# Performance work log

Measured on AMD Instinct MI355X. Metric: run time of the kernel, lower is better.

## Reference

```python
import jax, jax.numpy as jnp
import numpy as np

B = 32            # batch size
N = 100           # n_nodes (== MAX_N_NODES here)
MAXN = 100        # MAX_N_NODES
H = 256           # HIDDEN_DIM_FEATURES_EXTRACTOR
HA = 1024         # HIDDEN_DIM_ACTOR
HC = 512          # HIDDEN_DIM_CRITIC
K_ACTIVE = 5000   # exact number of active mask entries per batch element


def setup_inputs() -> dict:
    key = jax.random.key(0)
    ks = jax.random.split(key, 16)
    feat = jax.random.normal(ks[0], (B, N + 1, H), jnp.float32)
    # mask: exactly K_ACTIVE ones among N*N per batch row (dim == K for all rows)
    rng = np.random.default_rng(0)
    mask = np.zeros((B, N * N), np.float32)
    for i in range(B):
        mask[i, rng.choice(N * N, size=K_ACTIVE, replace=False)] = 1.0
    mask = jnp.asarray(mask).reshape(B, N, N)
    ext_mask = jnp.concatenate([jnp.zeros((B, 1, N), jnp.float32), mask], axis=1)  # [B, N+1, N]
    embedded_features = jnp.concatenate([feat, ext_mask], axis=2)  # [B, N+1, H+N]

    def lin(k, fi, fo):
        s = 1.0 / np.sqrt(fi)
        return (jax.random.uniform(k, (fi, fo), jnp.float32, -s, s),
                jax.random.uniform(jax.random.fold_in(k, 1), (fo,), jnp.float32, -s, s))

    aW1, ab1 = lin(ks[1], 3 * H, HA)
    aW2, ab2 = lin(ks[2], HA, HA)
    aW3, ab3 = lin(ks[3], HA, 1)
    cW1, cb1 = lin(ks[4], H, HC)
    cW2, cb2 = lin(ks[5], HC, HC)
    cW3, cb3 = lin(ks[6], HC, 1)
    return dict(embedded_features=embedded_features,
                aW1=aW1, ab1=ab1, aW2=aW2, ab2=ab2, aW3=aW3, ab3=ab3,
                cW1=cW1, cb1=cb1, cW2=cW2, cb2=cb2, cW3=cW3, cb3=cb3,
                K=K_ACTIVE)


def reference(embedded_features, aW1, ab1, aW2, ab2, aW3, ab3,
              cW1, cb1, cW2, cb2, cW3, cb3, K):
    # decompose features
    gn = embedded_features[:, :, :H]
    ext_mask = embedded_features[:, :, H:]
    g = gn[:, :1, :]                      # [B,1,H] graph embedding
    nodes = gn[:, 1:, :]                  # [B,N,H] node embeddings
    mask = ext_mask[:, 1:, :].reshape(B, -1)  # [B, N*N]

    # indexes of active pairs (stable top_k -> ascending indices among ones, like nonzero)
    _, idx = jax.lax.top_k(mask, K)       # [B,K] int32
    idx1 = idx // N
    idx2 = idx % N
    n1 = jnp.take_along_axis(nodes, idx1[:, :, None], axis=1)  # [B,K,H]
    n2 = jnp.take_along_axis(nodes, idx2[:, :, None], axis=1)  # [B,K,H]
    pairs = jnp.concatenate([jnp.broadcast_to(g, (B, K, H)), n1, n2], axis=-1)  # [B,K,3H]

    # actor MLP (tanh hidden activations)
    h = jnp.tanh(pairs @ aW1 + ab1)
    h = jnp.tanh(h @ aW2 + ab2)
    logits = h @ aW3 + ab3                # [B,K,1]
    pi = jax.nn.softmax(logits, axis=1)   # softmax over the K gathered pairs

    # scatter back into padded grid
    shaped = jnp.zeros((B, N * N), pi.dtype).at[jnp.arange(B)[:, None], idx].set(pi[..., 0])
    filled = jnp.zeros((B, MAXN, MAXN), pi.dtype).at[:, :N, :N].set(shaped.reshape(B, N, N))
    filled = filled.reshape(B, MAXN * MAXN)

    # critic MLP on graph embedding
    hv = jnp.tanh(g @ cW1 + cb1)
    hv = jnp.tanh(hv @ cW2 + cb2)
    value = hv @ cW3 + cb3                # [B,1,1]
    return filled, value
```

## Files before the change

kernel.cpp:

```cpp
#include <hip/hip_runtime.h>
#include <stdint.h>

#define AS1 __attribute__((address_space(1)))
#define AS3 __attribute__((address_space(3)))

typedef __bf16 bf16x8 __attribute__((ext_vector_type(8)));
typedef float  f32x4  __attribute__((ext_vector_type(4)));
typedef int    i32x4  __attribute__((ext_vector_type(4)));
typedef int    i32x8  __attribute__((ext_vector_type(8)));
typedef float  f32x16 __attribute__((ext_vector_type(16)));

__device__ __forceinline__ float tanh_fast(float x){
    float e = __expf(2.0f * x);
    return 1.0f - 2.0f * __builtin_amdgcn_rcpf(e + 1.0f);
}

__device__ __forceinline__ unsigned int cvt_pk_bf16(float lo, float hi){
    unsigned int r;
    asm("v_cvt_pk_bf16_f32 %0, %1, %2" : "=v"(r) : "v"(lo), "v"(hi));
    return r;
}
__device__ __forceinline__ unsigned short f2bf1(float f){
    return (unsigned short)(cvt_pk_bf16(f, f) & 0xffffu);
}

__device__ __forceinline__ float exp2_fast(float x){
#if defined(__has_builtin) && __has_builtin(__builtin_amdgcn_exp2f)
    return __builtin_amdgcn_exp2f(x);
#else
    float r; asm("v_exp_f32 %0, %1" : "=v"(r) : "v"(x)); return r;
#endif
}

__device__ __forceinline__ float q4s(float s){
    float a  = fabsf(s);
    float m1 = fmaf(a, 3.931945f, 0.0039260f);
    float m2 = fmaf(a, 3.428853f, 0.1414056f);
    float m3 = fmaf(a, 1.610679f, 1.3191011f);
    float g  = fminf(fminf(m1, m2), fminf(m3, 4.0f));
    return __builtin_copysignf(g, s);
}

template<int SEL>
__device__ __forceinline__ unsigned int pk4(unsigned int old, float a, float b){
#if defined(__has_builtin) && __has_builtin(__builtin_amdgcn_cvt_scalef32_pk_fp4_f32)
    return __builtin_amdgcn_cvt_scalef32_pk_fp4_f32(old, a, b, 1.0f, SEL);
#else
    float fa = fabsf(a), fb = fabsf(b);
    unsigned int ma = fa < 0.25f ? 0u : fa < 0.75f ? 1u : fa < 1.25f ? 2u :
                      fa < 1.75f ? 3u : fa < 2.5f  ? 4u : fa < 3.5f  ? 5u :
                      fa < 5.0f  ? 6u : 7u;
    unsigned int mb = fb < 0.25f ? 0u : fb < 0.75f ? 1u : fb < 1.25f ? 2u :
                      fb < 1.75f ? 3u : fb < 2.5f  ? 4u : fb < 3.5f  ? 5u :
                      fb < 5.0f  ? 6u : 7u;
    ma |= (a < 0.0f ? 8u : 0u); mb |= (b < 0.0f ? 8u : 0u);
    return old | ((ma | (mb << 4)) << (8 * SEL));
#endif
}

__device__ __forceinline__ i32x8 lo4(i32x4 a){
    return __builtin_shufflevector(a, a, 0, 1, 2, 3, -1, -1, -1, -1);
}

#define B2F(u, lo, hi) { lo = __uint_as_float((u) << 16); hi = __uint_as_float((u) & 0xffff0000u); }

__device__ __forceinline__ unsigned int mk4(uint4 qa, uint4 qb){
    float a0, a1, b0, b1; unsigned int dd = 0;
    B2F(qa.x, a0, a1); B2F(qb.x, b0, b1); dd = pk4<0>(dd, q4s(a0 + b0), q4s(a1 + b1));
    B2F(qa.y, a0, a1); B2F(qb.y, b0, b1); dd = pk4<1>(dd, q4s(a0 + b0), q4s(a1 + b1));
    B2F(qa.z, a0, a1); B2F(qb.z, b0, b1); dd = pk4<2>(dd, q4s(a0 + b0), q4s(a1 + b1));
    B2F(qa.w, a0, a1); B2F(qb.w, b0, b1); dd = pk4<3>(dd, q4s(a0 + b0), q4s(a1 + b1));
    return dd;
}
__device__ __forceinline__ i32x4 mkaf(uint4 a0, uint4 a1, uint4 a2, uint4 a3,
                                      uint4 b0, uint4 b1, uint4 b2, uint4 b3){
    i32x4 f = {(int)mk4(a0, b0), (int)mk4(a1, b1), (int)mk4(a2, b2), (int)mk4(a3, b3)};
    return f;
}

__global__ __launch_bounds__(256) void k_prep(
    const float* __restrict__ ef, const float* __restrict__ aW1, const float* __restrict__ ab1,
    const float* __restrict__ aW2,
    const float* __restrict__ cW1, const float* __restrict__ cb1,
    const float* __restrict__ cW2, const float* __restrict__ cb2,
    const float* __restrict__ cW3, const float* __restrict__ cb3,
    unsigned short* __restrict__ w1b, float* __restrict__ g1,
    int* __restrict__ pairs, unsigned char* __restrict__ w2b,
    float* __restrict__ out)
{
    __shared__ float gsl[256], h1[512], h2[512], wred[4];
    __shared__ int lcnt;
    int blk = blockIdx.x, t = threadIdx.x;

    if (blk < 256){
        int s = blk >> 7, cb = (blk >> 3) & 15, kt = blk & 7;
        int w = t >> 6, lane = t & 63, quad = lane >> 4, n = lane & 15;
        int c = cb * 64 + w * 16 + n;
        const float* src = aW1 + (size_t)(256 + s * 256 + kt * 32 + quad * 8) * 1024 + c;
        unsigned int d[4];
#pragma unroll
        for (int j = 0; j < 4; ++j)
            d[j] = cvt_pk_bf16(src[(size_t)(2*j) * 1024], src[(size_t)(2*j+1) * 1024]);
        *(uint4*)(w1b + (size_t)blk * 2048 + t * 8) = make_uint4(d[0], d[1], d[2], d[3]);
    } else if (blk < 384){
        int bi = blk - 256, b = bi >> 2, q = bi & 3;
        gsl[t] = ef[(size_t)b * 35956 + t];
        __syncthreads();
        int o = q * 256 + t;
        float s = ab1[o];
#pragma unroll 8
        for (int i = 0; i < 256; ++i)
            s = fmaf(gsl[i], aW1[(size_t)i * 1024 + o], s);
        g1[b * 1024 + o] = s;
    } else if (blk < 416){
        int b = blk - 384;
        gsl[t] = ef[(size_t)b * 35956 + t];
        __syncthreads();
        for (int o = t; o < 512; o += 256){
            float s0 = cb1[o], s1 = 0.f, s2 = 0.f, s3 = 0.f;
            const float* cp = cW1 + o;
#pragma unroll 8
            for (int i = 0; i < 256; i += 4){
                s0 = fmaf(gsl[i],     cp[(size_t)(i    ) * 512], s0);
                s1 = fmaf(gsl[i + 1], cp[(size_t)(i + 1) * 512], s1);
                s2 = fmaf(gsl[i + 2], cp[(size_t)(i + 2) * 512], s2);
                s3 = fmaf(gsl[i + 3], cp[(size_t)(i + 3) * 512], s3);
            }
            h1[o] = tanh_fast((s0 + s1) + (s2 + s3));
        }
        __syncthreads();
        for (int o = t; o < 512; o += 256){
            float s0 = cb2[o], s1 = 0.f, s2 = 0.f, s3 = 0.f;
            const float* cp = cW2 + o;
#pragma unroll 8
            for (int i = 0; i < 512; i += 4){
                s0 = fmaf(h1[i],     cp[(size_t)(i    ) * 512], s0);
                s1 = fmaf(h1[i + 1], cp[(size_t)(i + 1) * 512], s1);
                s2 = fmaf(h1[i + 2], cp[(size_t)(i + 2) * 512], s2);
                s3 = fmaf(h1[i + 3], cp[(size_t)(i + 3) * 512], s3);
            }
            h2[o] = tanh_fast((s0 + s1) + (s2 + s3));
        }
        __syncthreads();
        float p = h2[t] * cW3[t] + h2[t + 256] * cW3[t + 256];
        for (int m = 32; m >= 1; m >>= 1) p += __shfl_xor(p, m);
        if ((t & 63) == 0) wred[t >> 6] = p;
        __syncthreads();
        if (t == 0) out[320000 + b] = wred[0] + wred[1] + wred[2] + wred[3] + cb3[0];
    } else if (blk < 448){
        int b = blk - 416;
        int lane = t & 63;
        if (t == 0) lcnt = 0;
        __syncthreads();
        for (int i = 0; i < 40; ++i){
            int pos = i * 256 + t;
            bool valid = false;
            if (pos < 10000){
                int r = pos / 100, cc = pos - r * 100;
                valid = ef[(size_t)b * 35956 + (size_t)(1 + r) * 356 + 256 + cc] != 0.0f;
            }
            unsigned long long bal = __ballot(valid);
            int wbase;
            if (lane == 0) wbase = atomicAdd(&lcnt, __popcll(bal));
            wbase = __shfl(wbase, 0);
            if (valid){
                int o = wbase + __popcll(bal & ((1ull << lane) - 1ull));
                pairs[b * 5000 + o] = pos;
            }
        }
    } else if (blk < 576){
        int tid = (blk - 448) * 256 + t;
        int lane = tid & 63, kt = (tid >> 6) & 15, ct = tid >> 10;
        int lh = lane >> 5, n = lane & 31;
        const float* src = aW2 + (size_t)(kt * 64 + lh * 32) * 1024 + ct * 32 + n;
        unsigned int d[4] = {0u, 0u, 0u, 0u};
#pragma unroll
        for (int j = 0; j < 32; ++j){
            float a = src[(size_t)j * 1024] * 128.0f;
            float f = fabsf(a);
            unsigned int m = f < 0.25f ? 0u : f < 0.75f ? 1u : f < 1.25f ? 2u :
                             f < 1.75f ? 3u : f < 2.5f  ? 4u : f < 3.5f  ? 5u :
                             f < 5.0f  ? 6u : 7u;
            unsigned int nib = m | (a < 0.0f ? 8u : 0u);
            d[j >> 3] |= nib << (4 * (j & 7));
        }
        *(uint4*)(w2b + (size_t)(ct * 16 + kt) * 1024 + lane * 16) =
            make_uint4(d[0], d[1], d[2], d[3]);
    } else {
        int b = blk - 576;
        float4 z = make_float4(0.f, 0.f, 0.f, 0.f);
        float4* ob = (float4*)(out + (size_t)b * 10000);
        for (int j = t; j < 2500; j += 256) ob[j] = z;
    }
}

__global__ __launch_bounds__(256) void k_big(
    const float* __restrict__ ef, const unsigned short* __restrict__ w1b,
    const float* __restrict__ g1, unsigned short* __restrict__ P)
{
    __shared__ __align__(16) unsigned short an[112 * 264];
    int blk = blockIdx.x, t = threadIdx.x;
    int cb = blk & 15, b = blk >> 4;

    for (int it = 0; it < 25; ++it){
        int idx = it * 256 + t;
        int row = idx >> 6, c4 = idx & 63;
        const float* sp = ef + (size_t)b * 35956 + (size_t)(1 + row) * 356 + c4 * 4;
        float4 f = *(const float4*)sp;
        *(uint2*)(an + row * 264 + c4 * 4) =
            make_uint2(cvt_pk_bf16(f.x, f.y), cvt_pk_bf16(f.z, f.w));
    }
    for (int e = t; e < 3168; e += 256) an[26400 + e] = 0;
    __syncthreads();

    int w = t >> 6, lane = t & 63, quad = lane >> 4, n = lane & 15;
    int c = cb * 64 + w * 16 + n;
    bf16x8 bfr0[8], bfr1[8];
#pragma unroll
    for (int kt = 0; kt < 8; ++kt){
        uint4 q0 = *(const uint4*)(w1b + ((size_t)(      cb * 8 + kt) * 256 + t) * 8);
        uint4 q1 = *(const uint4*)(w1b + ((size_t)(128 + cb * 8 + kt) * 256 + t) * 8);
        bfr0[kt] = *(bf16x8*)&q0;
        bfr1[kt] = *(bf16x8*)&q1;
    }
    f32x4 acc0[7], acc1[7];
#pragma unroll
    for (int m = 0; m < 7; ++m){ f32x4 z = {0.f, 0.f, 0.f, 0.f}; acc0[m] = z; acc1[m] = z; }
#pragma unroll
    for (int kt = 0; kt < 8; ++kt){
#pragma unroll
        for (int m = 0; m < 7; ++m){
            const bf16x8* ap = (const bf16x8*)(an + (m * 16 + n) * 264 + kt * 32 + quad * 8);
            bf16x8 av = *ap;
            acc0[m] = __builtin_amdgcn_mfma_f32_16x16x32_bf16(av, bfr0[kt], acc0[m], 0, 0, 0);
            acc1[m] = __builtin_amdgcn_mfma_f32_16x16x32_bf16(av, bfr1[kt], acc1[m], 0, 0, 0);
        }
    }
    float addv = g1[b * 1024 + c];
    size_t base = (size_t)b * 102400;
#pragma unroll
    for (int m = 0; m < 7; ++m){
        int r0 = m * 16 + quad * 4;
#pragma unroll
        for (int r = 0; r < 4; ++r){
            int row = r0 + r;
            if (row < 100){
                P[base + (size_t)row * 1024 + c]           = f2bf1(acc0[m][r] + addv);
                P[3276800 + base + (size_t)row * 1024 + c] = f2bf1(acc1[m][r]);
            }
        }
    }
}

__global__ __launch_bounds__(256, 3) void k_main(
    const int* __restrict__ pairs,
    const unsigned short* __restrict__ P1, const unsigned short* __restrict__ P2,
    const unsigned char* __restrict__ w2b, const float* __restrict__ ab2,
    const float* __restrict__ aW3, float* __restrict__ logits)
{
    __shared__ __align__(16) unsigned char wbuf[2][16384];
    int t = threadIdx.x, w = t >> 6, lane = t & 63;
    int lrow = lane & 31, lh = lane >> 5;
    int soff = w * 4096 + lane * 16;
    int blk = blockIdx.x;
    int xcd = blk & 7, local = blk >> 3;
    int b = xcd + 8 * (local / 40);
    int tile = local - (local / 40) * 40;

    {
        const unsigned char* s = w2b + soff;
        unsigned char* d = &wbuf[0][0] + soff;
#pragma unroll
        for (int i = 0; i < 4; ++i)
            __builtin_amdgcn_global_load_lds((AS1 void*)(s + i * 1024),
                                             (AS3 void*)(d + i * 1024), 16, 0, 0);
    }

    int grow = tile * 128 + w * 32 + lrow;
    int pidx = pairs[b * 5000 + (grow < 5000 ? grow : 4999)];
    int i1 = pidx / 100, i2 = pidx - i1 * 100;
    const uint4* pa = (const uint4*)(P1 + (((size_t)(b * 100 + i1)) << 10)) + lh * 4;
    const uint4* pb = (const uint4*)(P2 + (((size_t)(b * 100 + i2)) << 10)) + lh * 4;

    i32x4 af4[16];
    uint4 A0, A1, A2, A3, B0, B1, B2, B3;
    uint4 C0, C1, C2, C3, D0, D1, D2, D3;
    A0 = pa[0]; A1 = pa[1]; A2 = pa[2]; A3 = pa[3];
    B0 = pb[0]; B1 = pb[1]; B2 = pb[2]; B3 = pb[3];
#pragma unroll
    for (int kh = 0; kh < 8; ++kh){
        int k0 = 2 * kh, k1 = k0 + 1;
        C0 = pa[k1*8+0]; C1 = pa[k1*8+1]; C2 = pa[k1*8+2]; C3 = pa[k1*8+3];
        D0 = pb[k1*8+0]; D1 = pb[k1*8+1]; D2 = pb[k1*8+2]; D3 = pb[k1*8+3];
        af4[k0] = mkaf(A0, A1, A2, A3, B0, B1, B2, B3);
        if (kh < 7){
            int k2 = k0 + 2;
            A0 = pa[k2*8+0]; A1 = pa[k2*8+1]; A2 = pa[k2*8+2]; A3 = pa[k2*8+3];
            B0 = pb[k2*8+0]; B1 = pb[k2*8+1]; B2 = pb[k2*8+2]; B3 = pb[k2*8+3];
        }
        af4[k1] = mkaf(C0, C1, C2, C3, D0, D1, D2, D3);
    }

    float prt[16];
#pragma unroll
    for (int r = 0; r < 16; ++r) prt[r] = 0.f;
    float sw3 = 0.f;
    f32x16 acc;

    for (int ct = 0; ct < 32; ++ct){
        __syncthreads();
        if (ct < 31){
            const unsigned char* sp = w2b + (size_t)(ct + 1) * 16384 + soff;
            unsigned char* d = &wbuf[(ct + 1) & 1][0] + soff;
#pragma unroll
            for (int i = 0; i < 4; ++i)
                __builtin_amdgcn_global_load_lds((AS1 void*)(sp + i * 1024),
                                                 (AS3 void*)(d + i * 1024), 16, 0, 0);
        }
#pragma unroll
        for (int r = 0; r < 16; ++r) acc[r] = 0.f;
        const unsigned char* bb = &wbuf[ct & 1][0] + lane * 16;
#pragma unroll
        for (int kt = 0; kt < 16; ++kt){
            uint4 q = *(const uint4*)(bb + kt * 1024);
            i32x4 bq = {(int)q.x, (int)q.y, (int)q.z, (int)q.w};
            acc = __builtin_amdgcn_mfma_scale_f32_32x32x64_f8f6f4(
                      lo4(af4[kt]), lo4(bq), acc, 4, 4, 0, 0x7D7D7D7D, 0, 0x78787878);
        }
        int cc = ct * 32 + lrow;
        float w3  = aW3[cc];
        float bc  = ab2[cc] * 2.8853900817779268f;
        float w3m = -2.0f * w3;
        sw3 += w3;
#pragma unroll
        for (int r = 0; r < 16; ++r){
            float a = fmaf(acc[r], 2.8853900817779268f, bc);
            float e = exp2_fast(a);
            prt[r] = fmaf(w3m, __builtin_amdgcn_rcpf(e + 1.0f), prt[r]);
        }
    }

#pragma unroll
    for (int r = 0; r < 16; ++r){
        float v = prt[r] + sw3;
        v += __shfl_xor(v, 1); v += __shfl_xor(v, 2); v += __shfl_xor(v, 4);
        v += __shfl_xor(v, 8); v += __shfl_xor(v, 16);
        if (lrow == 0){
            int row = (r & 3) + 8 * (r >> 2) + 4 * lh;
            int g = tile * 128 + w * 32 + row;
            if (g < 5000) logits[b * 5000 + g] = v;
        }
    }
}

__global__ void k_soft(const float* __restrict__ logits, const int* __restrict__ pairs,
                       float* __restrict__ out){
    int b = blockIdx.x, t = threadIdx.x;
    __shared__ float red[4];
    __shared__ float bmS, bsS;
    float* ob = out + (size_t)b * 10000;
    const float* lg = logits + b * 5000;
    float m = -1e30f;
    for (int j = t; j < 5000; j += 256) m = fmaxf(m, lg[j]);
    for (int s = 32; s >= 1; s >>= 1) m = fmaxf(m, __shfl_xor(m, s));
    if ((t & 63) == 0) red[t >> 6] = m;
    __syncthreads();
    if (t == 0) bmS = fmaxf(fmaxf(red[0], red[1]), fmaxf(red[2], red[3]));
    __syncthreads();
    float mm = bmS;
    float s = 0.f;
    for (int j = t; j < 5000; j += 256) s += __expf(lg[j] - mm);
    for (int k = 32; k >= 1; k >>= 1) s += __shfl_xor(s, k);
    if ((t & 63) == 0) red[t >> 6] = s;
    __syncthreads();
    if (t == 0) bsS = 1.0f / (red[0] + red[1] + red[2] + red[3]);
    __syncthreads();
    float inv = bsS;
    for (int j = t; j < 5000; j += 256){
        int pos = pairs[b * 5000 + j];
        ob[pos] = __expf(lg[j] - mm) * inv;
    }
}

extern "C" void kernel_launch(void* const* d_in, const int* in_sizes, int n_in,
                              void* d_out, int out_size, void* d_ws, size_t ws_size,
                              hipStream_t stream) {
    (void)in_sizes; (void)n_in; (void)out_size; (void)ws_size;
    const float* ef  = (const float*)d_in[0];
    const float* aW1 = (const float*)d_in[1];
    const float* ab1 = (const float*)d_in[2];
    const float* aW2 = (const float*)d_in[3];
    const float* ab2 = (const float*)d_in[4];
    const float* aW3 = (const float*)d_in[5];
    const float* cW1 = (const float*)d_in[7];
    const float* cb1 = (const float*)d_in[8];
    const float* cW2 = (const float*)d_in[9];
    const float* cb2 = (const float*)d_in[10];
    const float* cW3 = (const float*)d_in[11];
    const float* cb3 = (const float*)d_in[12];
    float* out = (float*)d_out;
    char* ws = (char*)d_ws;
    int*   pairs  = (int*)(ws + 0);
    float* logits = (float*)(ws + 640000);
    unsigned short* P1 = (unsigned short*)(ws + 1411072);
    unsigned short* P2 = (unsigned short*)(ws + 7964672);
    unsigned char*  w2b = (unsigned char*)(ws + 14518272);
    unsigned short* w1b = (unsigned short*)(ws + 15042560);
    float* g1     = (float*)(ws + 16091136);

    k_prep<<<608,  256, 0, stream>>>(ef, aW1, ab1, aW2, cW1, cb1, cW2, cb2, cW3, cb3,
                                     w1b, g1, pairs, w2b, out);
    k_big <<<512,  256, 0, stream>>>(ef, w1b, g1, P1);
    k_main<<<1280, 256, 0, stream>>>(pairs, P1, P2, w2b, ab2, aW3, logits);
    k_soft<<<32,   256, 0, stream>>>(logits, pairs, out);
}
```

Before: 285.4 us.

## Split fused gather-quantize-GEMM kernel into separate quantize and GEMM kernels

Splits the main kernel into two kernels. The first gathers the P1/P2 rows for each active pair, applies tanh and quantizes them to fp4 activation fragments in an 80 MB workspace buffer. The second streams those fragments straight into scaled MFMA with the double-buffered weights. The aim is to take the gather and quantization out of the GEMM inner loop so that kernel can run at higher occupancy. The cost is an extra launch and a large global write plus read of the fragments, and the path is only taken when the workspace is large enough.

```diff
diff --git a/kernel.cpp b/kernel.cpp
--- a/kernel.cpp
+++ b/kernel.cpp
@@ -248,6 +248,124 @@
                 P[base + (size_t)row * 1024 + c]           = f2bf1(acc0[m][r] + addv);
                 P[3276800 + base + (size_t)row * 1024 + c] = f2bf1(acc1[m][r]);
             }
+        }
+    }
+}
+
+__global__ __launch_bounds__(256) void k_quant(
+    const int* __restrict__ pairs,
+    const unsigned short* __restrict__ P1, const unsigned short* __restrict__ P2,
+    unsigned char* __restrict__ af4g)
+{
+    int t = threadIdx.x, w = t >> 6, lane = t & 63;
+    int lrow = lane & 31, lh = lane >> 5;
+    int blk = blockIdx.x;
+    int xcd = blk & 7, local = blk >> 3;
+    int b = xcd + 8 * (local / 40);
+    int tile = local - (local / 40) * 40;
+
+    int grow = tile * 128 + w * 32 + lrow;
+    int pidx = pairs[b * 5000 + (grow < 5000 ? grow : 4999)];
+    int i1 = pidx / 100, i2 = pidx - i1 * 100;
+    const uint4* pa = (const uint4*)(P1 + (((size_t)(b * 100 + i1)) << 10)) + lh * 4;
+    const uint4* pb = (const uint4*)(P2 + (((size_t)(b * 100 + i2)) << 10)) + lh * 4;
+    unsigned char* ob = af4g + (size_t)blk * 65536 + t * 16;
+
+    uint4 A0, A1, A2, A3, B0, B1, B2, B3;
+    uint4 C0, C1, C2, C3, D0, D1, D2, D3;
+    A0 = pa[0]; A1 = pa[1]; A2 = pa[2]; A3 = pa[3];
+    B0 = pb[0]; B1 = pb[1]; B2 = pb[2]; B3 = pb[3];
+#pragma unroll
+    for (int kh = 0; kh < 8; ++kh){
+        int k0 = 2 * kh, k1 = k0 + 1;
+        C0 = pa[k1*8+0]; C1 = pa[k1*8+1]; C2 = pa[k1*8+2]; C3 = pa[k1*8+3];
+        D0 = pb[k1*8+0]; D1 = pb[k1*8+1]; D2 = pb[k1*8+2]; D3 = pb[k1*8+3];
+        i32x4 f0 = mkaf(A0, A1, A2, A3, B0, B1, B2, B3);
+        *(i32x4*)(ob + (size_t)k0 * 4096) = f0;
+        if (kh < 7){
+            int k2 = k0 + 2;
+            A0 = pa[k2*8+0]; A1 = pa[k2*8+1]; A2 = pa[k2*8+2]; A3 = pa[k2*8+3];
+            B0 = pb[k2*8+0]; B1 = pb[k2*8+1]; B2 = pb[k2*8+2]; B3 = pb[k2*8+3];
+        }
+        i32x4 f1 = mkaf(C0, C1, C2, C3, D0, D1, D2, D3);
+        *(i32x4*)(ob + (size_t)k1 * 4096) = f1;
+    }
+}
+
+__global__ __launch_bounds__(256) void k_gemm(
+    const unsigned char* __restrict__ af4g,
+    const unsigned char* __restrict__ w2b, const float* __restrict__ ab2,
+    const float* __restrict__ aW3, float* __restrict__ logits)
+{
+    __shared__ __align__(16) unsigned char wbuf[2][16384];
+    int t = threadIdx.x, w = t >> 6, lane = t & 63;
+    int lrow = lane & 31, lh = lane >> 5;
+    int soff = w * 4096 + lane * 16;
+    int blk = blockIdx.x;
+    int xcd = blk & 7, local = blk >> 3;
+    int b = xcd + 8 * (local / 40);
+    int tile = local - (local / 40) * 40;
+    const unsigned char* ab = af4g + (size_t)blk * 65536 + t * 16;
+
+    {
+        const unsigned char* s = w2b + soff;
+        unsigned char* d = &wbuf[0][0] + soff;
+#pragma unroll
+        for (int i = 0; i < 4; ++i)
+            __builtin_amdgcn_global_load_lds((AS1 void*)(s + i * 1024),
+                                             (AS3 void*)(d + i * 1024), 16, 0, 0);
+    }
+
+    float prt[16];
+#pragma unroll
+    for (int r = 0; r < 16; ++r) prt[r] = 0.f;
+    float sw3 = 0.f;
+    f32x16 acc;
+
+    for (int ct = 0; ct < 32; ++ct){
+        __syncthreads();
+        if (ct < 31){
+            const unsigned char* sp = w2b + (size_t)(ct + 1) * 16384 + soff;
+            unsigned char* d = &wbuf[(ct + 1) & 1][0] + soff;
+#pragma unroll
+            for (int i = 0; i < 4; ++i)
+                __builtin_amdgcn_global_load_lds((AS1 void*)(sp + i * 1024),
+                                                 (AS3 void*)(d + i * 1024), 16, 0, 0);
+        }
+#pragma unroll
+        for (int r = 0; r < 16; ++r) acc[r] = 0.f;
+        const unsigned char* bb = &wbuf[ct & 1][0] + lane * 16;
+#pragma unroll
+        for (int kt = 0; kt < 16; ++kt){
+            uint4 fa = *(const uint4*)(ab + (size_t)kt * 4096);
+            i32x4 af = {(int)fa.x, (int)fa.y, (int)fa.z, (int)fa.w};
+            uint4 q = *(const uint4*)(bb + kt * 1024);
+            i32x4 bq = {(int)q.x, (int)q.y, (int)q.z, (int)q.w};
+            acc = __builtin_amdgcn_mfma_scale_f32_32x32x64_f8f6f4(
+                      lo4(af), lo4(bq), acc, 4, 4, 0, 0x7D7D7D7D, 0, 0x78787878);
+        }
+        int cc = ct * 32 + lrow;
+        float w3  = aW3[cc];
+        float bc  = ab2[cc] * 2.8853900817779268f;
+        float w3m = -2.0f * w3;
+        sw3 += w3;
+#pragma unroll
+        for (int r = 0; r < 16; ++r){
+            float a = fmaf(acc[r], 2.8853900817779268f, bc);
+            float e = exp2_fast(a);
+            prt[r] = fmaf(w3m, __builtin_amdgcn_rcpf(e + 1.0f), prt[r]);
+        }
+    }
+
+#pragma unroll
+    for (int r = 0; r < 16; ++r){
+        float v = prt[r] + sw3;
+        v += __shfl_xor(v, 1); v += __shfl_xor(v, 2); v += __shfl_xor(v, 4);
+        v += __shfl_xor(v, 8); v += __shfl_xor(v, 16);
+        if (lrow == 0){
+            int row = (r & 3) + 8 * (r >> 2) + 4 * lh;
+            int g = tile * 128 + w * 32 + row;
+            if (g < 5000) logits[b * 5000 + g] = v;
         }
     }
 }
@@ -385,7 +503,7 @@
 extern "C" void kernel_launch(void* const* d_in, const int* in_sizes, int n_in,
                               void* d_out, int out_size, void* d_ws, size_t ws_size,
                               hipStream_t stream) {
-    (void)in_sizes; (void)n_in; (void)out_size; (void)ws_size;
+    (void)in_sizes; (void)n_in; (void)out_size;
     const float* ef  = (const float*)d_in[0];
     const float* aW1 = (const float*)d_in[1];
     const float* ab1 = (const float*)d_in[2];
@@ -407,10 +525,17 @@
     unsigned char*  w2b = (unsigned char*)(ws + 14518272);
     unsigned short* w1b = (unsigned short*)(ws + 15042560);
     float* g1     = (float*)(ws + 16091136);
+    unsigned char* af4g = (unsigned char*)(ws + 16222208);
+    const size_t WS_NEED = 16222208ull + 83886080ull;
 
     k_prep<<<608,  256, 0, stream>>>(ef, aW1, ab1, aW2, cW1, cb1, cW2, cb2, cW3, cb3,
                                      w1b, g1, pairs, w2b, out);
     k_big <<<512,  256, 0, stream>>>(ef, w1b, g1, P1);
-    k_main<<<1280, 256, 0, stream>>>(pairs, P1, P2, w2b, ab2, aW3, logits);
+    if (ws_size >= WS_NEED){
+        k_quant<<<1280, 256, 0, stream>>>(pairs, P1, P2, af4g);
+        k_gemm <<<1280, 256, 0, stream>>>(af4g, w2b, ab2, aW3, logits);
+    } else {
+        k_main <<<1280, 256, 0, stream>>>(pairs, P1, P2, w2b, ab2, aW3, logits);
+    }
     k_soft<<<32,   256, 0, stream>>>(logits, pairs, out);
 }
```

Result: slower. 295.9 us (+3.7%).
